# Kernel tuning notes

Measured on AMD Instinct MI355X. Metric: run time of the kernel, lower is better.

Reference implementation:

```python
import jax, jax.numpy as jnp
import numpy as np

B, T, D, H, K, DEPTH = 2, 2048, 512, 8, 16, 3
EPS = 1e-5


def setup_inputs() -> dict:
    key = jax.random.key(0)
    ks = jax.random.split(key, 6)
    s = 0.02
    return {
        "x": jax.random.normal(ks[0], (B, T, D), jnp.float32),
        "ln1_s": jnp.ones((DEPTH, D), jnp.float32),
        "ln1_b": jnp.zeros((DEPTH, D), jnp.float32),
        "qkv_w": jax.random.normal(ks[1], (DEPTH, D, 3 * D), jnp.float32) * s,
        "proj_w": jax.random.normal(ks[2], (DEPTH, D, D), jnp.float32) * s,
        "proj_b": jnp.zeros((DEPTH, D), jnp.float32),
        "ln2_s": jnp.ones((DEPTH, D), jnp.float32),
        "ln2_b": jnp.zeros((DEPTH, D), jnp.float32),
        "w1": jax.random.normal(ks[3], (DEPTH, D, 4 * D), jnp.float32) * s,
        "b1": jnp.zeros((DEPTH, 4 * D), jnp.float32),
        "w2": jax.random.normal(ks[4], (DEPTH, 4 * D, D), jnp.float32) * s,
        "b2": jnp.zeros((DEPTH, D), jnp.float32),
    }


def _ln(x, s, b):
    m = x.mean(-1, keepdims=True)
    v = ((x - m) ** 2).mean(-1, keepdims=True)
    return (x - m) * jax.lax.rsqrt(v + EPS) * s + b


def _dilated_mask(t, dil):
    # allowed key j for query i: j = i - step*dil, step in [0, K), j >= 0
    i = jnp.arange(t)[:, None]
    j = jnp.arange(t)[None, :]
    diff = i - j
    ok = (diff >= 0) & (diff % dil == 0) & (diff < K * dil)
    return jnp.where(ok, 0.0, -jnp.inf).astype(jnp.float32)


def reference(x, ln1_s, ln1_b, qkv_w, proj_w, proj_b, ln2_s, ln2_b, w1, b1, w2, b2):
    hd = D // H
    scale = hd ** -0.5
    for d in range(DEPTH):
        dil = 2 ** d
        h = _ln(x, ln1_s[d], ln1_b[d])
        qkv = (h @ qkv_w[d]).reshape(B, T, 3, H, hd).transpose(2, 0, 3, 1, 4)
        q, k, v = qkv[0], qkv[1], qkv[2]  # each (B,H,T,hd)
        attn = jnp.einsum('bhid,bhjd->bhij', q, k) * scale + _dilated_mask(T, dil)
        o = jnp.einsum('bhij,bhjd->bhid', jax.nn.softmax(attn, axis=-1), v)
        o = o.transpose(0, 2, 1, 3).reshape(B, T, D) @ proj_w[d] + proj_b[d]
        x = x + o
        h = _ln(x, ln2_s[d], ln2_b[d])
        x = x + (jax.nn.gelu(h @ w1[d] + b1[d], approximate=False) @ w2[d] + b2[d])
    return x
```

## Files before the change

kernel.cpp:

```cpp
#include <hip/hip_runtime.h>
#include <math.h>

#define TSEQ   2048
#define DM     512
#define NH     8
#define HD     64
#define KATT   16
#define NDEPTH 3
#define MROWS  4096

typedef __attribute__((ext_vector_type(8))) short bf16x8;
typedef __attribute__((ext_vector_type(8))) unsigned short u16x8;
typedef __attribute__((ext_vector_type(4))) float f32x4;

static __device__ __forceinline__ unsigned short f2b(float f) {
    unsigned int u = __float_as_uint(f);
    unsigned int r = (u + 0x7fffu + ((u >> 16) & 1u)) >> 16;
    return (unsigned short)r;
}
static __device__ __forceinline__ float b2f(unsigned short s) {
    return __uint_as_float((unsigned int)s << 16);
}

static __device__ __forceinline__ void load_lds16(const void* g, void* l) {
    __builtin_amdgcn_global_load_lds(
        (const __attribute__((address_space(1))) unsigned int*)g,
        (__attribute__((address_space(3))) unsigned int*)l, 16, 0, 0);
}

static __device__ __forceinline__ float fast_erf(float x) {
    const float a  = fabsf(x);
    const float t  = 1.0f / (1.0f + 0.3275911f * a);
    const float p  = t * (0.254829592f + t * (-0.284496736f +
                     t * (1.421413741f + t * (-1.453152027f + t * 1.061405429f))));
    const float e  = __expf(-a * a);
    const float r  = 1.0f - p * e;
    return __builtin_copysignf(r, x);
}

__global__ __launch_bounds__(256) void prep_kernel(
    const float* __restrict__ qkv_w, const float* __restrict__ proj_w,
    const float* __restrict__ w1,    const float* __restrict__ w2,
    unsigned short* __restrict__ qkvT, unsigned short* __restrict__ projT,
    unsigned short* __restrict__ w1T,  unsigned short* __restrict__ w2T,
    const float* __restrict__ x, const float* __restrict__ sc,
    const float* __restrict__ bi, unsigned short* __restrict__ h)
{
    __shared__ float tile[32][33];
    int id = blockIdx.x;
    const int tid = threadIdx.x;

    if (id < 9216) {
        const float* W; unsigned short* Wt; int Kd, Nd;
        if (id < 2304)      { W = qkv_w;  Wt = qkvT;  Kd = 512;  Nd = 1536; }
        else if (id < 3072) { W = proj_w; Wt = projT; Kd = 512;  Nd = 512;  id -= 2304; }
        else if (id < 6144) { W = w1;     Wt = w1T;   Kd = 512;  Nd = 2048; id -= 3072; }
        else                { W = w2;     Wt = w2T;   Kd = 2048; Nd = 512;  id -= 6144; }
        const int nt = Nd >> 5, per = nt * (Kd >> 5);
        const int d = id / per, rem = id % per;
        const int k0 = (rem / nt) * 32, n0 = (rem % nt) * 32;

        const size_t off = (size_t)d * Kd * Nd;
        const float* Wd = W + off;
        unsigned short* Wtd = Wt + off;
        const int tx = tid & 31, ty = tid >> 5;
#pragma unroll
        for (int r = 0; r < 32; r += 8)
            tile[ty + r][tx] = Wd[(size_t)(k0 + ty + r) * Nd + (n0 + tx)];
        __syncthreads();
#pragma unroll
        for (int r = 0; r < 32; r += 8)
            Wtd[(size_t)(n0 + ty + r) * Kd + (k0 + tx)] = f2b(tile[tx][ty + r]);
        return;
    }

    const int wid  = (id - 9216) * 4 + (tid >> 6);
    const int lane = tid & 63;
    const float* xr = x + (size_t)wid * DM;
    const float4 v0 = *(const float4*)&xr[lane * 4];
    const float4 v1 = *(const float4*)&xr[256 + lane * 4];
    float s = v0.x + v0.y + v0.z + v0.w + v1.x + v1.y + v1.z + v1.w;
    float q = v0.x*v0.x + v0.y*v0.y + v0.z*v0.z + v0.w*v0.w
            + v1.x*v1.x + v1.y*v1.y + v1.z*v1.z + v1.w*v1.w;
#pragma unroll
    for (int off = 32; off; off >>= 1) {
        s += __shfl_xor(s, off, 64);
        q += __shfl_xor(q, off, 64);
    }
    const float mean = s * (1.0f / DM);
    const float var  = q * (1.0f / DM) - mean * mean;
    const float rs   = rsqrtf(var + 1e-5f);
    unsigned short* hr = h + (size_t)wid * DM;
    const int c0 = lane * 4, c1 = 256 + lane * 4;
    ushort4 o0, o1;
    o0.x = f2b((v0.x - mean) * rs * sc[c0+0] + bi[c0+0]);
    o0.y = f2b((v0.y - mean) * rs * sc[c0+1] + bi[c0+1]);
    o0.z = f2b((v0.z - mean) * rs * sc[c0+2] + bi[c0+2]);
    o0.w = f2b((v0.w - mean) * rs * sc[c0+3] + bi[c0+3]);
    o1.x = f2b((v1.x - mean) * rs * sc[c1+0] + bi[c1+0]);
    o1.y = f2b((v1.y - mean) * rs * sc[c1+1] + bi[c1+1]);
    o1.z = f2b((v1.z - mean) * rs * sc[c1+2] + bi[c1+2]);
    o1.w = f2b((v1.w - mean) * rs * sc[c1+3] + bi[c1+3]);
    *(ushort4*)&hr[c0] = o0;
    *(ushort4*)&hr[c1] = o1;
}

__global__ __launch_bounds__(256) void attn_kernel(
    const unsigned short* __restrict__ qh, const unsigned short* __restrict__ kh,
    const unsigned short* __restrict__ vh, unsigned short* __restrict__ o, int dil)
{
    const int blk  = blockIdx.x;
    const int tile = blk & (TSEQ / 16 - 1);
    const int bh   = blk >> 7;
    const int b    = bh >> 3, hh = bh & 7;
    const int t0   = tile * 16;
    const int tid  = threadIdx.x;
    const int wave = tid >> 6, lane = tid & 63;
    const int tq   = wave * 4 + (lane >> 4);
    const int s    = lane & 15;
    const int t    = t0 + tq;
    const size_t slab = ((size_t)hh * MROWS + (size_t)b * TSEQ) * HD;

    const int R    = 15 * dil + 16;
    const int base = t0 - 15 * dil;

    __shared__ unsigned short ks[76 * 64];
    __shared__ unsigned short vs[76 * 64];
    __shared__ unsigned short qs[16 * 64];
    __shared__ float p_lds[16][17];

    for (int c = tid; c < R * 8; c += 256) {
        const int r = c >> 3, cs = c & 7;
        const int sr = max(base + r, 0);
        const int ps = ((cs + r + (r >> 2)) & 7) * 8;
        const size_t g = slab + (size_t)sr * HD + cs * 8;
        *(u16x8*)&ks[r * 64 + ps] = *(const u16x8*)(kh + g);
        *(u16x8*)&vs[r * 64 + ps] = *(const u16x8*)(vh + g);
    }
    if (tid < 128) {
        const int r = tid >> 3, cs = tid & 7;
        *(u16x8*)&qs[r * 64 + cs * 8] =
            *(const u16x8*)(qh + slab + (size_t)(t0 + r) * HD + cs * 8);
    }
    __syncthreads();

    const bool valid = (t - s * dil) >= 0;
    const int  kidx  = tq + 15 * dil - s * dil;
    float dot = 0.0f;
#pragma unroll
    for (int j = 0; j < 8; j++) {
        const u16x8 kk = *(const u16x8*)&ks[kidx * 64 + (((j + kidx + (kidx >> 2)) & 7) * 8)];
        const u16x8 qq = *(const u16x8*)&qs[tq * 64 + j * 8];
#pragma unroll
        for (int e = 0; e < 8; e++) dot += b2f(qq[e]) * b2f(kk[e]);
    }
    const float sc = valid ? dot * 0.125f : -1e30f;
    float m = sc;
#pragma unroll
    for (int off = 1; off < 16; off <<= 1) m = fmaxf(m, __shfl_xor(m, off, 64));
    const float p = expf(sc - m);
    float l = p;
#pragma unroll
    for (int off = 1; off < 16; off <<= 1) l += __shfl_xor(l, off, 64);
    p_lds[tq][s] = p / l;
    __syncthreads();

#pragma unroll
    for (int qi = 0; qi < 4; qi++) {
        const int qq = qi * 4 + wave;
        float acc = 0.0f;
#pragma unroll
        for (int ss = 0; ss < KATT; ss++) {
            const int idx = qq + 15 * dil - ss * dil;
            const float pw = p_lds[qq][ss];
            const int ps = (((lane >> 3) + idx + (idx >> 2)) & 7);
            acc += pw * b2f(vs[idx * 64 + ps * 8 + (lane & 7)]);
        }
        o[(size_t)(b * TSEQ + (t0 + qq)) * DM + (size_t)hh * HD + lane] = f2b(acc);
    }
}

template<int EPI, int TN>
__global__ __launch_bounds__(256) void gemm_kernel(
    const unsigned short* __restrict__ A,
    const unsigned short* __restrict__ Bt,
    const float* __restrict__ bias,
    unsigned short* __restrict__ outp,
    unsigned short* __restrict__ outb,
    unsigned short* __restrict__ outq,
    unsigned short* __restrict__ outk,
    unsigned short* __restrict__ outv,
    int N, int K, int Kslice, size_t zstride)
{
    constexpr int FN = TN / 32;
    constexpr int CA = 2;
    constexpr int CB = TN / 64;
    const int tid  = threadIdx.x;
    const int wave = tid >> 6, lane = tid & 63;
    const int bm = blockIdx.y * 128;
    const int bn = blockIdx.x * TN;
    const int wm = (wave >> 1) * 64;
    const int wn = (wave & 1) * (TN / 2);
    const int ml = lane & 15, quad = lane >> 4;
    const int kbeg = blockIdx.z * Kslice;

    __shared__ unsigned short As[2][128 * 32];
    __shared__ unsigned short Bs[2][TN * 32];

    f32x4 acc[4][FN] = {};

    const int rr = lane >> 2, ss = lane & 3;
    const int cc = ((ss - (rr >> 1)) & 3) * 8;
    const unsigned short* Aa[CA];
    const unsigned short* Bb[CB];
#pragma unroll
    for (int j = 0; j < CA; j++)
        Aa[j] = A + (size_t)(bm + (wave * CA + j) * 16 + rr) * K + kbeg + cc;
#pragma unroll
    for (int j = 0; j < CB; j++)
        Bb[j] = Bt + (size_t)(bn + (wave * CB + j) * 16 + rr) * K + kbeg + cc;

    const int fslot = ((quad + (ml >> 1)) & 3) * 8;

#pragma unroll
    for (int j = 0; j < CA; j++)
        load_lds16(Aa[j], &As[0][(wave * CA + j) * 512]);
#pragma unroll
    for (int j = 0; j < CB; j++)
        load_lds16(Bb[j], &Bs[0][(wave * CB + j) * 512]);
    __syncthreads();

    const int steps = Kslice >> 5;
    for (int s = 0; s < steps; s++) {
        const int cur = s & 1, nxt = cur ^ 1;
        const bool more = (s + 1 < steps);
        if (more) {
            const int k0 = (s + 1) * 32;
#pragma unroll
            for (int j = 0; j < CA; j++)
                load_lds16(Aa[j] + k0, &As[nxt][(wave * CA + j) * 512]);
#pragma unroll
            for (int j = 0; j < CB; j++)
                load_lds16(Bb[j] + k0, &Bs[nxt][(wave * CB + j) * 512]);
        }

        bf16x8 af[4], bfr[FN];
#pragma unroll
        for (int i = 0; i < 4; i++)
            af[i] = *(const bf16x8*)&As[cur][(wm + i * 16 + ml) * 32 + fslot];
#pragma unroll
        for (int j = 0; j < FN; j++)
            bfr[j] = *(const bf16x8*)&Bs[cur][(wn + j * 16 + ml) * 32 + fslot];

#pragma unroll
        for (int i = 0; i < 4; i++)
#pragma unroll
            for (int j = 0; j < FN; j++)
                acc[i][j] = __builtin_amdgcn_mfma_f32_16x16x32_bf16(
                    af[i], bfr[j], acc[i][j], 0, 0, 0);

        if (more) __syncthreads();
    }

    unsigned short* op = outp + (size_t)blockIdx.z * zstride;
#pragma unroll
    for (int i = 0; i < 4; i++)
#pragma unroll
        for (int j = 0; j < FN; j++)
#pragma unroll
            for (int r = 0; r < 4; r++) {
                const int row = bm + wm + i * 16 + quad * 4 + r;
                const int col = bn + wn + j * 16 + ml;
                const float v = acc[i][j][r];
                if (EPI == 0) {
                    op[(size_t)row * N + col] = f2b(v);
                } else if (EPI == 2) {
                    const float u = v + bias[col];
                    const float g = 0.5f * u * (1.0f + fast_erf(u * 0.70710678118654752f));
                    outb[(size_t)row * N + col] = f2b(g);
                } else {
                    const int which = col >> 9;
                    const int hh = (col & 511) >> 6;
                    const int dim = col & 63;
                    unsigned short* dst =
                        which == 0 ? outq : (which == 1 ? outk : outv);
                    dst[((size_t)hh * MROWS + row) * HD + dim] = f2b(v);
                }
            }
}

template<bool DO_LN, int Z>
__global__ __launch_bounds__(256) void reduce_kernel(
    const float* __restrict__ xin,
    const unsigned short* __restrict__ part,
    const float* __restrict__ bias,
    const float* __restrict__ lns, const float* __restrict__ lnb,
    float* __restrict__ xout, unsigned short* __restrict__ h)
{
    const int wid  = blockIdx.x * 4 + (threadIdx.x >> 6);
    const int lane = threadIdx.x & 63;
    const int c0 = lane * 4, c1 = 256 + lane * 4;
    const size_t ro = (size_t)wid * DM;

    float4 a0 = *(const float4*)&xin[ro + c0];
    float4 a1 = *(const float4*)&xin[ro + c1];
#pragma unroll
    for (int z = 0; z < Z; z++) {
        const unsigned short* p = part + (size_t)z * (MROWS * (size_t)DM) + ro;
        const ushort4 p0 = *(const ushort4*)&p[c0];
        const ushort4 p1 = *(const ushort4*)&p[c1];
        a0.x += b2f(p0.x); a0.y += b2f(p0.y); a0.z += b2f(p0.z); a0.w += b2f(p0.w);
        a1.x += b2f(p1.x); a1.y += b2f(p1.y); a1.z += b2f(p1.z); a1.w += b2f(p1.w);
    }
    a0.x += bias[c0+0]; a0.y += bias[c0+1]; a0.z += bias[c0+2]; a0.w += bias[c0+3];
    a1.x += bias[c1+0]; a1.y += bias[c1+1]; a1.z += bias[c1+2]; a1.w += bias[c1+3];

    *(float4*)&xout[ro + c0] = a0;
    *(float4*)&xout[ro + c1] = a1;

    if (DO_LN) {
        float s = a0.x + a0.y + a0.z + a0.w + a1.x + a1.y + a1.z + a1.w;
        float q = a0.x*a0.x + a0.y*a0.y + a0.z*a0.z + a0.w*a0.w
                + a1.x*a1.x + a1.y*a1.y + a1.z*a1.z + a1.w*a1.w;
#pragma unroll
        for (int off = 32; off; off >>= 1) {
            s += __shfl_xor(s, off, 64);
            q += __shfl_xor(q, off, 64);
        }
        const float mean = s * (1.0f / DM);
        const float var  = q * (1.0f / DM) - mean * mean;
        const float rs   = rsqrtf(var + 1e-5f);
        unsigned short* hr = h + ro;
        ushort4 o0, o1;
        o0.x = f2b((a0.x - mean) * rs * lns[c0+0] + lnb[c0+0]);
        o0.y = f2b((a0.y - mean) * rs * lns[c0+1] + lnb[c0+1]);
        o0.z = f2b((a0.z - mean) * rs * lns[c0+2] + lnb[c0+2]);
        o0.w = f2b((a0.w - mean) * rs * lns[c0+3] + lnb[c0+3]);
        o1.x = f2b((a1.x - mean) * rs * lns[c1+0] + lnb[c1+0]);
        o1.y = f2b((a1.y - mean) * rs * lns[c1+1] + lnb[c1+1]);
        o1.z = f2b((a1.z - mean) * rs * lns[c1+2] + lnb[c1+2]);
        o1.w = f2b((a1.w - mean) * rs * lns[c1+3] + lnb[c1+3]);
        *(ushort4*)&hr[c0] = o0;
        *(ushort4*)&hr[c1] = o1;
    }
}

extern "C" void kernel_launch(void* const* d_in, const int* in_sizes, int n_in,
                              void* d_out, int out_size, void* d_ws, size_t ws_size,
                              hipStream_t stream)
{
    (void)in_sizes; (void)n_in; (void)out_size; (void)ws_size;
    const float* x_in   = (const float*)d_in[0];
    const float* ln1_s  = (const float*)d_in[1];
    const float* ln1_b  = (const float*)d_in[2];
    const float* qkv_w  = (const float*)d_in[3];
    const float* proj_w = (const float*)d_in[4];
    const float* proj_b = (const float*)d_in[5];
    const float* ln2_s  = (const float*)d_in[6];
    const float* ln2_b  = (const float*)d_in[7];
    const float* w1     = (const float*)d_in[8];
    const float* b1     = (const float*)d_in[9];
    const float* w2     = (const float*)d_in[10];
    const float* b2     = (const float*)d_in[11];

    char* ws = (char*)d_ws;
    float*          xbuf = (float*)(ws);
    unsigned short* qhb  = (unsigned short*)(ws + 8388608);
    unsigned short* khb  = (unsigned short*)(ws + 12582912);
    unsigned short* vhb  = (unsigned short*)(ws + 16777216);
    unsigned short* ubuf = (unsigned short*)(ws + 33554432);
    unsigned short* hbuf = (unsigned short*)(ws + 50331648);
    unsigned short* obuf = (unsigned short*)(ws + 54525952);
    unsigned short* part = (unsigned short*)(ws + 58720256);
    unsigned short* qkvT = (unsigned short*)(ws + 92274688);
    unsigned short* projT= (unsigned short*)(ws + 96993280);
    unsigned short* w1T  = (unsigned short*)(ws + 98566144);
    unsigned short* w2T  = (unsigned short*)(ws + 104857600);

    const size_t ZS = (size_t)MROWS * DM;

    prep_kernel<<<10240, 256, 0, stream>>>(
        qkv_w, proj_w, w1, w2, qkvT, projT, w1T, w2T,
        x_in, ln1_s, ln1_b, hbuf);

    for (int d = 0; d < NDEPTH; d++) {
        const int dil = 1 << d;
        const float* xin = (d == 0) ? x_in : xbuf;

        gemm_kernel<3, 64><<<dim3(1536/64, MROWS/128, 1), 256, 0, stream>>>(
            hbuf, qkvT + (size_t)d * 1536 * 512, nullptr, nullptr, nullptr,
            qhb, khb, vhb, 1536, 512, 512, 0);
        attn_kernel<<<2 * NH * (TSEQ / 16), 256, 0, stream>>>(qhb, khb, vhb, obuf, dil);
        gemm_kernel<0, 64><<<dim3(512/64, MROWS/128, 2), 256, 0, stream>>>(
            obuf, projT + (size_t)d * 512 * 512, nullptr, part, nullptr,
            nullptr, nullptr, nullptr, 512, 512, 256, ZS);
        reduce_kernel<true, 2><<<MROWS / 4, 256, 0, stream>>>(
            xin, part, proj_b + d * DM, ln2_s + d * DM, ln2_b + d * DM,
            xbuf, hbuf);
        gemm_kernel<2, 128><<<dim3(2048/128, MROWS/128, 1), 256, 0, stream>>>(
            hbuf, w1T + (size_t)d * 2048 * 512, b1 + d * 2048, nullptr, ubuf,
            nullptr, nullptr, nullptr, 2048, 512, 512, 0);
        gemm_kernel<0, 128><<<dim3(512/128, MROWS/128, 4), 256, 0, stream>>>(
            ubuf, w2T + (size_t)d * 512 * 2048, nullptr, part, nullptr,
            nullptr, nullptr, nullptr, 512, 2048, 512, ZS);
        if (d < NDEPTH - 1) {
            reduce_kernel<true, 4><<<MROWS / 4, 256, 0, stream>>>(
                xbuf, part, b2 + d * DM, ln1_s + (d+1) * DM, ln1_b + (d+1) * DM,
                xbuf, hbuf);
        } else {
            reduce_kernel<false, 4><<<MROWS / 4, 256, 0, stream>>>(
                xbuf, part, b2 + d * DM, nullptr, nullptr,
                (float*)d_out, nullptr);
        }
    }
}
```

Measured before the change: 390.1 us.

## Remap workgroups XCD-aware and deepen GEMM K-step per barrier

Block indices in the attention and GEMM kernels are remapped so that consecutive logical tiles go to the same XCD (block id modulo 8 is spread across contiguous ranges), aiming for better L2 reuse of shared A/B rows and K/V slabs. The GEMM grids become 1D with explicit gx/gy decoding. A PK template parameter loads two 32-wide K chunks per pipeline stage for the QKV and proj GEMMs, halving barrier count at the cost of doubled LDS. It assumes grid sizes are divisible by 8.

New measurement: 362.6 us. -7.0%, faster.

```diff
diff --git a/kernel.cpp b/kernel.cpp
--- a/kernel.cpp
+++ b/kernel.cpp
@@ -109,9 +109,10 @@
     const unsigned short* __restrict__ qh, const unsigned short* __restrict__ kh,
     const unsigned short* __restrict__ vh, unsigned short* __restrict__ o, int dil)
 {
-    const int blk  = blockIdx.x;
-    const int tile = blk & (TSEQ / 16 - 1);
-    const int bh   = blk >> 7;
+    const int nwg = gridDim.x;
+    const int wg  = (blockIdx.x & 7) * (nwg >> 3) + (blockIdx.x >> 3);
+    const int tile = wg & (TSEQ / 16 - 1);
+    const int bh   = wg >> 7;
     const int b    = bh >> 3, hh = bh & 7;
     const int t0   = tile * 16;
     const int tid  = threadIdx.x;
@@ -180,7 +181,7 @@
     }
 }
 
-template<int EPI, int TN>
+template<int EPI, int TN, int PK>
 __global__ __launch_bounds__(256) void gemm_kernel(
     const unsigned short* __restrict__ A,
     const unsigned short* __restrict__ Bt,
@@ -190,22 +191,29 @@
     unsigned short* __restrict__ outq,
     unsigned short* __restrict__ outk,
     unsigned short* __restrict__ outv,
-    int N, int K, int Kslice, size_t zstride)
+    int N, int K, int Kslice, size_t zstride, int gx, int gy)
 {
     constexpr int FN = TN / 32;
     constexpr int CA = 2;
     constexpr int CB = TN / 64;
     const int tid  = threadIdx.x;
     const int wave = tid >> 6, lane = tid & 63;
-    const int bm = blockIdx.y * 128;
-    const int bn = blockIdx.x * TN;
+
+    const int nwg = gridDim.x;
+    const int wg  = (blockIdx.x & 7) * (nwg >> 3) + (blockIdx.x >> 3);
+    const int bxi = wg % gx;
+    const int byi = (wg / gx) % gy;
+    const int bzi = wg / (gx * gy);
+
+    const int bm = byi * 128;
+    const int bn = bxi * TN;
     const int wm = (wave >> 1) * 64;
     const int wn = (wave & 1) * (TN / 2);
     const int ml = lane & 15, quad = lane >> 4;
-    const int kbeg = blockIdx.z * Kslice;
-
-    __shared__ unsigned short As[2][128 * 32];
-    __shared__ unsigned short Bs[2][TN * 32];
+    const int kbeg = bzi * Kslice;
+
+    __shared__ unsigned short As[2 * PK][128 * 32];
+    __shared__ unsigned short Bs[2 * PK][TN * 32];
 
     f32x4 acc[4][FN] = {};
 
@@ -223,46 +231,55 @@
     const int fslot = ((quad + (ml >> 1)) & 3) * 8;
 
 #pragma unroll
-    for (int j = 0; j < CA; j++)
-        load_lds16(Aa[j], &As[0][(wave * CA + j) * 512]);
-#pragma unroll
-    for (int j = 0; j < CB; j++)
-        load_lds16(Bb[j], &Bs[0][(wave * CB + j) * 512]);
+    for (int p = 0; p < PK; p++) {
+#pragma unroll
+        for (int j = 0; j < CA; j++)
+            load_lds16(Aa[j] + p * 32, &As[p][(wave * CA + j) * 512]);
+#pragma unroll
+        for (int j = 0; j < CB; j++)
+            load_lds16(Bb[j] + p * 32, &Bs[p][(wave * CB + j) * 512]);
+    }
     __syncthreads();
 
-    const int steps = Kslice >> 5;
+    const int steps = Kslice / (32 * PK);
     for (int s = 0; s < steps; s++) {
-        const int cur = s & 1, nxt = cur ^ 1;
+        const int cb = (s & 1) * PK, nb = cb ^ PK;
         const bool more = (s + 1 < steps);
         if (more) {
-            const int k0 = (s + 1) * 32;
-#pragma unroll
-            for (int j = 0; j < CA; j++)
-                load_lds16(Aa[j] + k0, &As[nxt][(wave * CA + j) * 512]);
-#pragma unroll
-            for (int j = 0; j < CB; j++)
-                load_lds16(Bb[j] + k0, &Bs[nxt][(wave * CB + j) * 512]);
+#pragma unroll
+            for (int p = 0; p < PK; p++) {
+                const int k0 = ((s + 1) * PK + p) * 32;
+#pragma unroll
+                for (int j = 0; j < CA; j++)
+                    load_lds16(Aa[j] + k0, &As[nb + p][(wave * CA + j) * 512]);
+#pragma unroll
+                for (int j = 0; j < CB; j++)
+                    load_lds16(Bb[j] + k0, &Bs[nb + p][(wave * CB + j) * 512]);
+            }
         }
 
-        bf16x8 af[4], bfr[FN];
-#pragma unroll
-        for (int i = 0; i < 4; i++)
-            af[i] = *(const bf16x8*)&As[cur][(wm + i * 16 + ml) * 32 + fslot];
-#pragma unroll
-        for (int j = 0; j < FN; j++)
-            bfr[j] = *(const bf16x8*)&Bs[cur][(wn + j * 16 + ml) * 32 + fslot];
-
-#pragma unroll
-        for (int i = 0; i < 4; i++)
+#pragma unroll
+        for (int p = 0; p < PK; p++) {
+            bf16x8 af[4], bfr[FN];
+#pragma unroll
+            for (int i = 0; i < 4; i++)
+                af[i] = *(const bf16x8*)&As[cb + p][(wm + i * 16 + ml) * 32 + fslot];
 #pragma unroll
             for (int j = 0; j < FN; j++)
-                acc[i][j] = __builtin_amdgcn_mfma_f32_16x16x32_bf16(
-                    af[i], bfr[j], acc[i][j], 0, 0, 0);
+                bfr[j] = *(const bf16x8*)&Bs[cb + p][(wn + j * 16 + ml) * 32 + fslot];
+
+#pragma unroll
+            for (int i = 0; i < 4; i++)
+#pragma unroll
+                for (int j = 0; j < FN; j++)
+                    acc[i][j] = __builtin_amdgcn_mfma_f32_16x16x32_bf16(
+                        af[i], bfr[j], acc[i][j], 0, 0, 0);
+        }
 
         if (more) __syncthreads();
     }
 
-    unsigned short* op = outp + (size_t)blockIdx.z * zstride;
+    unsigned short* op = outp + (size_t)bzi * zstride;
 #pragma unroll
     for (int i = 0; i < 4; i++)
 #pragma unroll
@@ -387,22 +404,22 @@
         const int dil = 1 << d;
         const float* xin = (d == 0) ? x_in : xbuf;
 
-        gemm_kernel<3, 64><<<dim3(1536/64, MROWS/128, 1), 256, 0, stream>>>(
+        gemm_kernel<3, 64, 2><<<768, 256, 0, stream>>>(
             hbuf, qkvT + (size_t)d * 1536 * 512, nullptr, nullptr, nullptr,
-            qhb, khb, vhb, 1536, 512, 512, 0);
+            qhb, khb, vhb, 1536, 512, 512, 0, 24, 32);
         attn_kernel<<<2 * NH * (TSEQ / 16), 256, 0, stream>>>(qhb, khb, vhb, obuf, dil);
-        gemm_kernel<0, 64><<<dim3(512/64, MROWS/128, 2), 256, 0, stream>>>(
+        gemm_kernel<0, 64, 2><<<512, 256, 0, stream>>>(
             obuf, projT + (size_t)d * 512 * 512, nullptr, part, nullptr,
-            nullptr, nullptr, nullptr, 512, 512, 256, ZS);
+            nullptr, nullptr, nullptr, 512, 512, 256, ZS, 8, 32);
         reduce_kernel<true, 2><<<MROWS / 4, 256, 0, stream>>>(
             xin, part, proj_b + d * DM, ln2_s + d * DM, ln2_b + d * DM,
             xbuf, hbuf);
-        gemm_kernel<2, 128><<<dim3(2048/128, MROWS/128, 1), 256, 0, stream>>>(
+        gemm_kernel<2, 128, 1><<<512, 256, 0, stream>>>(
             hbuf, w1T + (size_t)d * 2048 * 512, b1 + d * 2048, nullptr, ubuf,
-            nullptr, nullptr, nullptr, 2048, 512, 512, 0);
-        gemm_kernel<0, 128><<<dim3(512/128, MROWS/128, 4), 256, 0, stream>>>(
+            nullptr, nullptr, nullptr, 2048, 512, 512, 0, 16, 32);
+        gemm_kernel<0, 128, 1><<<512, 256, 0, stream>>>(
             ubuf, w2T + (size_t)d * 512 * 2048, nullptr, part, nullptr,
-            nullptr, nullptr, nullptr, 512, 2048, 512, ZS);
+            nullptr, nullptr, nullptr, 512, 2048, 512, ZS, 4, 32);
         if (d < NDEPTH - 1) {
             reduce_kernel<true, 4><<<MROWS / 4, 256, 0, stream>>>(
                 xbuf, part, b2 + d * DM, ln1_s + (d+1) * DM, ln1_b + (d+1) * DM,
```
